# Kernel tuning notes

Measured on AMD Instinct MI355X. Metric: run time of the kernel, lower is better.

The kernel has to match this reference:

```python
import jax, jax.numpy as jnp
import numpy as np

EMBED_DIM = 1024
SEQ_LEN = 4096
NUM_HEADS = 16
HEAD_DIM = EMBED_DIM // NUM_HEADS
FREQ_BINS = SEQ_LEN // 2 + 1  # 2049
LN_EPS = 1e-5


def setup_inputs() -> dict:
    key = jax.random.key(0)
    ks = jax.random.split(key, 12)
    B = 4
    x = jax.random.normal(ks[0], (B, SEQ_LEN, EMBED_DIM), dtype=jnp.float32)
    # LayerNorm affine params
    ln_w = jnp.ones((EMBED_DIM,), dtype=jnp.float32)
    ln_b = jnp.zeros((EMBED_DIM,), dtype=jnp.float32)
    # spectral base filter / bias: (H, freq_bins, 1)
    base_filter = jax.random.normal(ks[1], (NUM_HEADS, FREQ_BINS, 1), dtype=jnp.float32)
    base_bias = jax.random.normal(ks[2], (NUM_HEADS, FREQ_BINS, 1), dtype=jnp.float32) - 0.1
    # adaptive MLP (depth=2, width=embed_dim): D -> D -> D -> H*freq*2, relu hidden
    out_size = NUM_HEADS * FREQ_BINS * 2
    s0 = 1.0 / np.sqrt(EMBED_DIM)
    w0 = jax.random.uniform(ks[3], (EMBED_DIM, EMBED_DIM), jnp.float32, -s0, s0)
    b0 = jax.random.uniform(ks[4], (EMBED_DIM,), jnp.float32, -s0, s0)
    w1 = jax.random.uniform(ks[5], (EMBED_DIM, EMBED_DIM), jnp.float32, -s0, s0)
    b1 = jax.random.uniform(ks[6], (EMBED_DIM,), jnp.float32, -s0, s0)
    w2 = jax.random.uniform(ks[7], (EMBED_DIM, out_size), jnp.float32, -s0, s0)
    b2 = jax.random.uniform(ks[8], (out_size,), jnp.float32, -s0, s0)
    return {"x": x, "ln_w": ln_w, "ln_b": ln_b,
            "base_filter": base_filter, "base_bias": base_bias,
            "w0": w0, "b0": b0, "w1": w1, "b1": b1, "w2": w2, "b2": b2}


def _complex_activation(z):
    mag = jnp.abs(z)
    scale = jax.nn.gelu(mag) / (mag + 1e-6)
    return z * scale


def reference(x, ln_w, ln_b, base_filter, base_bias, w0, b0, w1, b1, w2, b2):
    B, N, D = x.shape  # N == SEQ_LEN, D == EMBED_DIM
    # pre-norm LayerNorm over last dim
    mu = x.mean(axis=-1, keepdims=True)
    var = x.var(axis=-1, keepdims=True)
    x_norm = (x - mu) / jnp.sqrt(var + LN_EPS) * ln_w + ln_b
    # split heads: (B, H, N, head_dim)
    x_heads = x_norm.reshape(B, N, NUM_HEADS, HEAD_DIM).transpose(0, 2, 1, 3)
    F_fft = jnp.fft.rfft(x_heads, axis=2)  # (B, H, freq, head_dim), complex
    # adaptive params from mean-pooled context
    context = x_norm.mean(axis=1)  # (B, D)
    h = jax.nn.relu(context @ w0 + b0)
    h = jax.nn.relu(h @ w1 + b1)
    adapt = h @ w2 + b2  # (B, H*freq*2)
    adapt = adapt.reshape(B, NUM_HEADS, FREQ_BINS, 2)
    adaptive_scale = adapt[..., 0:1]
    adaptive_bias = adapt[..., 1:2]
    effective_filter = base_filter * (1.0 + adaptive_scale)  # (B, H, freq, 1)
    effective_bias = base_bias + adaptive_bias
    F_mod = F_fft * effective_filter + effective_bias
    F_nl = _complex_activation(F_mod)
    x_filt = jnp.fft.irfft(F_nl, n=SEQ_LEN, axis=2)  # (B, H, N, head_dim)
    x_filt = x_filt.transpose(0, 2, 1, 3).reshape(B, SEQ_LEN, EMBED_DIM)
    return x_filt  # dropout is identity (inference / rate 0)
```

## Files before the change

kernel.cpp:

```cpp
#include <hip/hip_runtime.h>
#include <hip/hip_fp16.h>
#include <math.h>

#define B_ 4
#define N_ 4096
#define D_ 1024
#define H_ 16
#define HD_ 64
#define FB_ 2049

typedef unsigned short ushort_t;
typedef unsigned int uint_t;

__device__ __forceinline__ float2 cmul(float2 a, float2 b) {
    return make_float2(a.x*b.x - a.y*b.y, a.x*b.y + a.y*b.x);
}
__device__ __forceinline__ float2 cadd(float2 a, float2 b){return make_float2(a.x+b.x,a.y+b.y);}
__device__ __forceinline__ float2 csub(float2 a, float2 b){return make_float2(a.x-b.x,a.y-b.y);}
__device__ __forceinline__ float2 cconj(float2 a){return make_float2(a.x,-a.y);}
__device__ __forceinline__ float2 addi(float2 a, float2 b){return make_float2(a.x-b.y, a.y+b.x);}
__device__ __forceinline__ float2 subi(float2 a, float2 b){return make_float2(a.x+b.y, a.y-b.x);}

__device__ __forceinline__ float gelu_t(float m) {
    float u = 0.7978845608028654f * (m + 0.044715f * m * m * m);
    float e = __expf(-2.0f * u);
    float th = (1.0f - e) / (1.0f + e);
    return 0.5f * m * (1.0f + th);
}
__device__ __forceinline__ float2 cact(float2 z) {
    float m = sqrtf(z.x*z.x + z.y*z.y);
    float s = gelu_t(m) / (m + 1e-6f);
    return make_float2(z.x*s, z.y*s);
}

__device__ __forceinline__ ushort_t f2h(float f) {
    __half h = __float2half_rn(f);
    return *reinterpret_cast<ushort_t*>(&h);
}
__device__ __forceinline__ float h2f(ushort_t u) {
    __half h = *reinterpret_cast<__half*>(&u);
    return __half2float(h);
}
__device__ __forceinline__ uint_t pk2(float a, float b) {
    return (uint_t)f2h(a) | ((uint_t)f2h(b) << 16);
}
__device__ __forceinline__ float lo_f(uint_t u){ return h2f((ushort_t)(u & 0xffffu)); }
__device__ __forceinline__ float hi_f(uint_t u){ return h2f((ushort_t)(u >> 16)); }

#define IX(e) ((e) + ((e) >> 4))

__device__ __forceinline__ int rev12(int p) {
    return ((p & 7) << 9) | (((p >> 3) & 7) << 6) | (((p >> 6) & 7) << 3) | ((p >> 9) & 7);
}

__global__ __launch_bounds__(256) void k_normT(const float* __restrict__ x,
                                               const float* __restrict__ lnw,
                                               const float* __restrict__ lnb,
                                               ushort_t* __restrict__ xt,
                                               float* __restrict__ cpart) {
    __shared__ ushort_t lds16[32 * 1032];
    uint_t* lds32 = (uint_t*)lds16;
    int blk = blockIdx.x;
    int b = blk >> 7, chunk = blk & 127;
    int n0 = chunk << 5;
    int lane = threadIdx.x & 63, w = threadIdx.x >> 6;
    const float4* lw4 = (const float4*)lnw;
    const float4* lb4 = (const float4*)lnb;
    float4 W0 = lw4[lane], W1 = lw4[lane+64], W2 = lw4[lane+128], W3 = lw4[lane+192];
    float4 G0 = lb4[lane], G1 = lb4[lane+64], G2 = lb4[lane+128], G3 = lb4[lane+192];

    for (int j = 0; j < 8; j++) {
        int r = (w << 3) + j;
        const float4* xr = (const float4*)(x + ((size_t)b * N_ + n0 + r) * D_);
        float4 v0 = xr[lane], v1 = xr[lane+64], v2 = xr[lane+128], v3 = xr[lane+192];
        float s = v0.x+v0.y+v0.z+v0.w + v1.x+v1.y+v1.z+v1.w
                + v2.x+v2.y+v2.z+v2.w + v3.x+v3.y+v3.z+v3.w;
        float q = v0.x*v0.x+v0.y*v0.y+v0.z*v0.z+v0.w*v0.w
                + v1.x*v1.x+v1.y*v1.y+v1.z*v1.z+v1.w*v1.w
                + v2.x*v2.x+v2.y*v2.y+v2.z*v2.z+v2.w*v2.w
                + v3.x*v3.x+v3.y*v3.y+v3.z*v3.z+v3.w*v3.w;
        for (int o = 1; o < 64; o <<= 1) { s += __shfl_xor(s, o); q += __shfl_xor(q, o); }
        float mu = s * (1.0f / D_);
        float rstd = rsqrtf(q * (1.0f / D_) - mu * mu + 1e-5f);
        int base = r * 516 + 2 * lane;
        lds32[base]       = pk2((v0.x-mu)*rstd*W0.x+G0.x, (v0.y-mu)*rstd*W0.y+G0.y);
        lds32[base + 1]   = pk2((v0.z-mu)*rstd*W0.z+G0.z, (v0.w-mu)*rstd*W0.w+G0.w);
        lds32[base + 128] = pk2((v1.x-mu)*rstd*W1.x+G1.x, (v1.y-mu)*rstd*W1.y+G1.y);
        lds32[base + 129] = pk2((v1.z-mu)*rstd*W1.z+G1.z, (v1.w-mu)*rstd*W1.w+G1.w);
        lds32[base + 256] = pk2((v2.x-mu)*rstd*W2.x+G2.x, (v2.y-mu)*rstd*W2.y+G2.y);
        lds32[base + 257] = pk2((v2.z-mu)*rstd*W2.z+G2.z, (v2.w-mu)*rstd*W2.w+G2.w);
        lds32[base + 384] = pk2((v3.x-mu)*rstd*W3.x+G3.x, (v3.y-mu)*rstd*W3.y+G3.y);
        lds32[base + 385] = pk2((v3.z-mu)*rstd*W3.z+G3.z, (v3.w-mu)*rstd*W3.w+G3.w);
    }
    __syncthreads();
    for (int half = 0; half < 2; half++) {
        int dp = threadIdx.x + (half << 8);
        float cs_e = 0.f, cs_o = 0.f;
        uint_t ce[16], co[16];
        #pragma unroll
        for (int i = 0; i < 16; i++) {
            uint_t w0 = lds32[(2*i) * 516 + dp];
            uint_t w1 = lds32[(2*i+1) * 516 + dp];
            ce[i] = (w0 & 0xffffu) | (w1 << 16);
            co[i] = (w0 >> 16) | (w1 & 0xffff0000u);
            cs_e += lo_f(w0) + lo_f(w1);
            cs_o += hi_f(w0) + hi_f(w1);
        }
        int de = dp * 2;
        uint4* dste = (uint4*)(xt + ((size_t)(b * 1024 + de)) * 4096 + n0);
        dste[0] = make_uint4(ce[0], ce[1], ce[2], ce[3]);
        dste[1] = make_uint4(ce[4], ce[5], ce[6], ce[7]);
        dste[2] = make_uint4(ce[8], ce[9], ce[10], ce[11]);
        dste[3] = make_uint4(ce[12], ce[13], ce[14], ce[15]);
        uint4* dsto = (uint4*)(xt + ((size_t)(b * 1024 + de + 1)) * 4096 + n0);
        dsto[0] = make_uint4(co[0], co[1], co[2], co[3]);
        dsto[1] = make_uint4(co[4], co[5], co[6], co[7]);
        dsto[2] = make_uint4(co[8], co[9], co[10], co[11]);
        dsto[3] = make_uint4(co[12], co[13], co[14], co[15]);
        ((float2*)(cpart + ((size_t)(b * 128 + chunk)) * D_))[dp] = make_float2(cs_e, cs_o);
    }
}

__global__ __launch_bounds__(256) void k_ctx(const float* __restrict__ cpart,
                                             float* __restrict__ ctx) {
    int id = blockIdx.x * 256 + threadIdx.x;
    int b = id >> 10, d = id & 1023;
    float s = 0.f;
    const float* p = cpart + (size_t)b * 128 * D_ + d;
    #pragma unroll 8
    for (int g = 0; g < 128; g++) s += p[g * D_];
    ctx[id] = s * (1.0f / N_);
}

__global__ __launch_bounds__(256) void k_mlp_part(const float* __restrict__ in,
                                                  const float* __restrict__ w,
                                                  float* __restrict__ part) {
    __shared__ float li[4 * 256];
    int ks = blockIdx.y;
    for (int i = threadIdx.x; i < 1024; i += 256) {
        int b = i >> 8, kk = i & 255;
        li[i] = in[b * 1024 + ks * 256 + kk];
    }
    __syncthreads();
    int col = blockIdx.x * 64 + (threadIdx.x & 63);
    int b = threadIdx.x >> 6;
    const float* wp = w + (size_t)(ks * 256) * 1024 + col;
    const float* ip = li + b * 256;
    float acc = 0.f;
    #pragma unroll 8
    for (int k = 0; k < 256; k++) acc = fmaf(ip[k], wp[(size_t)k * 1024], acc);
    part[((size_t)ks * 4 + b) * 1024 + col] = acc;
}

__global__ __launch_bounds__(256) void k_mlp_part2(const float* __restrict__ part,
                                                   const float* __restrict__ bias,
                                                   const float* __restrict__ w,
                                                   float* __restrict__ part2) {
    __shared__ float li[4 * 256];
    int ks = blockIdx.y;
    for (int i = threadIdx.x; i < 1024; i += 256) {
        int b = i >> 8, kk = (i & 255) + ks * 256;
        float v = part[b * 1024 + kk] + part[4096 + b * 1024 + kk] +
                  part[8192 + b * 1024 + kk] + part[12288 + b * 1024 + kk] + bias[kk];
        li[i] = fmaxf(v, 0.f);
    }
    __syncthreads();
    int col = blockIdx.x * 64 + (threadIdx.x & 63);
    int b = threadIdx.x >> 6;
    const float* wp = w + (size_t)(ks * 256) * 1024 + col;
    const float* ip = li + b * 256;
    float acc = 0.f;
    #pragma unroll 8
    for (int k = 0; k < 256; k++) acc = fmaf(ip[k], wp[(size_t)k * 1024], acc);
    part2[((size_t)ks * 4 + b) * 1024 + col] = acc;
}

__global__ __launch_bounds__(256) void k_adapt_part(const float* __restrict__ part2,
                                                    const float* __restrict__ b1,
                                                    const float* __restrict__ w2,
                                                    float* __restrict__ part3) {
    __shared__ float lh[4 * 128];
    int ks = blockIdx.y;
    for (int i = threadIdx.x; i < 512; i += 256) {
        int b = i >> 7, kk = (i & 127) + ks * 128;
        float v = part2[b * 1024 + kk] + part2[4096 + b * 1024 + kk] +
                  part2[8192 + b * 1024 + kk] + part2[12288 + b * 1024 + kk] + b1[kk];
        lh[i] = fmaxf(v, 0.f);
    }
    __syncthreads();
    int j4 = blockIdx.x * 1024 + threadIdx.x * 4;
    if (j4 < 65568) {
        float a0x=0,a0y=0,a0z=0,a0w=0, a1x=0,a1y=0,a1z=0,a1w=0;
        float a2x=0,a2y=0,a2z=0,a2w=0, a3x=0,a3y=0,a3z=0,a3w=0;
        const float* wp = w2 + (size_t)(ks * 128) * 65568 + j4;
        #pragma unroll 4
        for (int k = 0; k < 128; k++) {
            float4 wv = *(const float4*)(wp + (size_t)k * 65568);
            float h0 = lh[k], h1 = lh[128 + k], h2 = lh[256 + k], h3 = lh[384 + k];
            a0x = fmaf(h0, wv.x, a0x); a0y = fmaf(h0, wv.y, a0y);
            a0z = fmaf(h0, wv.z, a0z); a0w = fmaf(h0, wv.w, a0w);
            a1x = fmaf(h1, wv.x, a1x); a1y = fmaf(h1, wv.y, a1y);
            a1z = fmaf(h1, wv.z, a1z); a1w = fmaf(h1, wv.w, a1w);
            a2x = fmaf(h2, wv.x, a2x); a2y = fmaf(h2, wv.y, a2y);
            a2z = fmaf(h2, wv.z, a2z); a2w = fmaf(h2, wv.w, a2w);
            a3x = fmaf(h3, wv.x, a3x); a3y = fmaf(h3, wv.y, a3y);
            a3z = fmaf(h3, wv.z, a3z); a3w = fmaf(h3, wv.w, a3w);
        }
        float* p3 = part3 + (size_t)ks * 4 * 65568 + j4;
        *(float4*)(p3)              = make_float4(a0x, a0y, a0z, a0w);
        *(float4*)(p3 + 65568)      = make_float4(a1x, a1y, a1z, a1w);
        *(float4*)(p3 + 2 * 65568)  = make_float4(a2x, a2y, a2z, a2w);
        *(float4*)(p3 + 3 * 65568)  = make_float4(a3x, a3y, a3z, a3w);
    }
}

__global__ __launch_bounds__(256) void k_eff(const float* __restrict__ part3,
                                             const float* __restrict__ b2,
                                             const float* __restrict__ bfilt,
                                             const float* __restrict__ bbias,
                                             float2* __restrict__ eff) {
    int p = blockIdx.x * 256 + threadIdx.x;
    if (p >= 32784) return;
    int h = p / 2049, f = p % 2049;
    float bf = bfilt[p], bb = bbias[p];
    float sc0 = b2[2 * p], bi0 = b2[2 * p + 1];
    #pragma unroll
    for (int b = 0; b < 4; b++) {
        float sc = sc0, bi = bi0;
        #pragma unroll
        for (int s = 0; s < 8; s++) {
            const float* q = part3 + ((size_t)s * 4 + b) * 65568 + 2 * p;
            sc += q[0]; bi += q[1];
        }
        eff[((size_t)b * H_ + h) * FB_ + f] = make_float2(bf * (1.0f + sc), bb + bi);
    }
}

template<int M, int SH, bool TW>
__device__ __forceinline__ void dif_stage(float2* buf, const float2* tw, int t) {
    const float s2 = 0.70710678118654752f;
    int j = t & (M - 1);
    int base = 8 * t - 7 * j;
    float2 u0 = buf[IX(base)];
    float2 u1 = buf[IX(base + M)];
    float2 u2 = buf[IX(base + 2*M)];
    float2 u3 = buf[IX(base + 3*M)];
    float2 u4 = buf[IX(base + 4*M)];
    float2 u5 = buf[IX(base + 5*M)];
    float2 u6 = buf[IX(base + 6*M)];
    float2 u7 = buf[IX(base + 7*M)];
    float2 a0 = cadd(u0,u4), a1 = csub(u0,u4), a2 = cadd(u2,u6), a3 = csub(u2,u6);
    float2 E0 = cadd(a0,a2), E1 = subi(a1,a3), E2 = csub(a0,a2), E3 = addi(a1,a3);
    float2 c0 = cadd(u1,u5), c1 = csub(u1,u5), c2 = cadd(u3,u7), c3 = csub(u3,u7);
    float2 O0 = cadd(c0,c2), O1 = subi(c1,c3), O2 = csub(c0,c2), O3 = addi(c1,c3);
    float2 R1 = make_float2(s2*(O1.x + O1.y), s2*(O1.y - O1.x));
    float2 R2 = make_float2(O2.y, -O2.x);
    float2 R3 = make_float2(s2*(O3.y - O3.x), -s2*(O3.x + O3.y));
    float2 X0 = cadd(E0,O0), X4 = csub(E0,O0);
    float2 X1 = cadd(E1,R1), X5 = csub(E1,R1);
    float2 X2 = cadd(E2,R2), X6 = csub(E2,R2);
    float2 X3 = cadd(E3,R3), X7 = csub(E3,R3);
    buf[IX(base)] = X0;
    if (TW) {
        float2 w1 = tw[IX(j << SH)];
        float2 w = w1;
        buf[IX(base + M)]   = cmul(w, X1); w = cmul(w, w1);
        buf[IX(base + 2*M)] = cmul(w, X2); w = cmul(w, w1);
        buf[IX(base + 3*M)] = cmul(w, X3); w = cmul(w, w1);
        buf[IX(base + 4*M)] = cmul(w, X4); w = cmul(w, w1);
        buf[IX(base + 5*M)] = cmul(w, X5); w = cmul(w, w1);
        buf[IX(base + 6*M)] = cmul(w, X6); w = cmul(w, w1);
        buf[IX(base + 7*M)] = cmul(w, X7);
    } else {
        buf[IX(base + M)]   = X1;
        buf[IX(base + 2*M)] = X2;
        buf[IX(base + 3*M)] = X3;
        buf[IX(base + 4*M)] = X4;
        buf[IX(base + 5*M)] = X5;
        buf[IX(base + 6*M)] = X6;
        buf[IX(base + 7*M)] = X7;
    }
}

template<int M, int SH, bool TW>
__device__ __forceinline__ void dit_stage(float2* buf, const float2* tw, int t) {
    const float s2 = 0.70710678118654752f;
    int j = t & (M - 1);
    int base = 8 * t - 7 * j;
    float2 u0 = buf[IX(base)];
    float2 u1, u2, u3, u4, u5, u6, u7;
    if (TW) {
        float2 w1 = cconj(tw[IX(j << SH)]);
        float2 w = w1;
        u1 = cmul(w, buf[IX(base + M)]);   w = cmul(w, w1);
        u2 = cmul(w, buf[IX(base + 2*M)]); w = cmul(w, w1);
        u3 = cmul(w, buf[IX(base + 3*M)]); w = cmul(w, w1);
        u4 = cmul(w, buf[IX(base + 4*M)]); w = cmul(w, w1);
        u5 = cmul(w, buf[IX(base + 5*M)]); w = cmul(w, w1);
        u6 = cmul(w, buf[IX(base + 6*M)]); w = cmul(w, w1);
        u7 = cmul(w, buf[IX(base + 7*M)]);
    } else {
        u1 = buf[IX(base + M)];
        u2 = buf[IX(base + 2*M)];
        u3 = buf[IX(base + 3*M)];
        u4 = buf[IX(base + 4*M)];
        u5 = buf[IX(base + 5*M)];
        u6 = buf[IX(base + 6*M)];
        u7 = buf[IX(base + 7*M)];
    }
    float2 a0 = cadd(u0,u4), a1 = csub(u0,u4), a2 = cadd(u2,u6), a3 = csub(u2,u6);
    float2 E0 = cadd(a0,a2), E1 = addi(a1,a3), E2 = csub(a0,a2), E3 = subi(a1,a3);
    float2 c0 = cadd(u1,u5), c1 = csub(u1,u5), c2 = cadd(u3,u7), c3 = csub(u3,u7);
    float2 O0 = cadd(c0,c2), O1 = addi(c1,c3), O2 = csub(c0,c2), O3 = subi(c1,c3);
    float2 R1 = make_float2(s2*(O1.x - O1.y),  s2*(O1.x + O1.y));
    float2 R2 = make_float2(-O2.y, O2.x);
    float2 R3 = make_float2(-s2*(O3.x + O3.y), s2*(O3.x - O3.y));
    buf[IX(base)]       = cadd(E0,O0);
    buf[IX(base + 4*M)] = csub(E0,O0);
    buf[IX(base + M)]   = cadd(E1,R1);
    buf[IX(base + 5*M)] = csub(E1,R1);
    buf[IX(base + 2*M)] = cadd(E2,R2);
    buf[IX(base + 6*M)] = csub(E2,R2);
    buf[IX(base + 3*M)] = cadd(E3,R3);
    buf[IX(base + 7*M)] = csub(E3,R3);
}

__global__ __launch_bounds__(512, 6) void k_fftmod(ushort_t* __restrict__ xt,
                                                   const float2* __restrict__ eff) {
    __shared__ float2 buf[4352];
    __shared__ float2 tw[544];
    int t = threadIdx.x;
    int sig0 = blockIdx.x * 2;
    int b = sig0 >> 10;
    int h = (sig0 & 1023) >> 6;
    const float2* ef = eff + ((size_t)b * H_ + h) * FB_;
    ushort_t* xs = xt + (size_t)sig0 * 4096;

    {
        float sv, cv;
        __sincosf(-(float)M_PI * (float)t * (1.0f / 2048.0f), &sv, &cv);
        tw[IX(t)] = make_float2(cv, sv);
    }
    {
        const uint4* pa = (const uint4*)xs;
        const uint4* pb = pa + 512;
        uint4 ua = pa[t], ub = pb[t];
        int n = t << 3;
        buf[IX(n+0)] = make_float2(lo_f(ua.x), lo_f(ub.x));
        buf[IX(n+1)] = make_float2(hi_f(ua.x), hi_f(ub.x));
        buf[IX(n+2)] = make_float2(lo_f(ua.y), lo_f(ub.y));
        buf[IX(n+3)] = make_float2(hi_f(ua.y), hi_f(ub.y));
        buf[IX(n+4)] = make_float2(lo_f(ua.z), lo_f(ub.z));
        buf[IX(n+5)] = make_float2(hi_f(ua.z), hi_f(ub.z));
        buf[IX(n+6)] = make_float2(lo_f(ua.w), lo_f(ub.w));
        buf[IX(n+7)] = make_float2(hi_f(ua.w), hi_f(ub.w));
    }
    __syncthreads();

    dif_stage<512, 0, true >(buf, tw, t); __syncthreads();
    dif_stage<64,  3, true >(buf, tw, t); __syncthreads();
    dif_stage<8,   6, true >(buf, tw, t); __syncthreads();
    dif_stage<1,   0, false>(buf, tw, t); __syncthreads();

    if (t == 0) {
        float2 Z = buf[IX(0)];
        float2 e0 = ef[0];
        float Av = Z.x * e0.x + e0.y;
        float Bv = Z.y * e0.x + e0.y;
        float ma = fabsf(Av); Av *= gelu_t(ma) / (ma + 1e-6f);
        float mb = fabsf(Bv); Bv *= gelu_t(mb) / (mb + 1e-6f);
        buf[IX(0)] = make_float2(Av, Bv);
    }
    #pragma unroll
    for (int ii = 0; ii < 4; ii++) {
        int k = 1 + t + (ii << 9);
        if (k == 2048) {
            float2 Z = buf[IX(4)];
            float2 eN = ef[2048];
            float Av = Z.x * eN.x + eN.y;
            float Bv = Z.y * eN.x + eN.y;
            float ma = fabsf(Av); Av *= gelu_t(ma) / (ma + 1e-6f);
            float mb = fabsf(Bv); Bv *= gelu_t(mb) / (mb + 1e-6f);
            buf[IX(4)] = make_float2(Av, Bv);
        } else {
            int pk = rev12(k);
            int pq = rev12(4096 - k);
            float2 Zk = buf[IX(pk)], Zq = buf[IX(pq)];
            float2 A  = make_float2(0.5f*(Zk.x + Zq.x), 0.5f*(Zk.y - Zq.y));
            float2 Bc = make_float2(0.5f*(Zk.y + Zq.y), 0.5f*(Zq.x - Zk.x));
            float2 e = ef[k];
            float2 Ap = make_float2(A.x * e.x + e.y,  A.y * e.x);
            float2 Bp = make_float2(Bc.x * e.x + e.y, Bc.y * e.x);
            Ap = cact(Ap); Bp = cact(Bp);
            buf[IX(pk)] = make_float2(Ap.x - Bp.y, Ap.y + Bp.x);
            buf[IX(pq)] = make_float2(Ap.x + Bp.y, Bp.x - Ap.y);
        }
    }
    __syncthreads();

    dit_stage<1,   0, false>(buf, tw, t); __syncthreads();
    dit_stage<8,   6, true >(buf, tw, t); __syncthreads();
    dit_stage<64,  3, true >(buf, tw, t); __syncthreads();
    dit_stage<512, 0, true >(buf, tw, t); __syncthreads();

    {
        const float sc = 1.0f / 4096.0f;
        int n = t << 3;
        float2 z0 = buf[IX(n+0)], z1 = buf[IX(n+1)], z2 = buf[IX(n+2)], z3 = buf[IX(n+3)];
        float2 z4 = buf[IX(n+4)], z5 = buf[IX(n+5)], z6 = buf[IX(n+6)], z7 = buf[IX(n+7)];
        uint4 oa, ob;
        oa.x = pk2(z0.x*sc, z1.x*sc); oa.y = pk2(z2.x*sc, z3.x*sc);
        oa.z = pk2(z4.x*sc, z5.x*sc); oa.w = pk2(z6.x*sc, z7.x*sc);
        ob.x = pk2(z0.y*sc, z1.y*sc); ob.y = pk2(z2.y*sc, z3.y*sc);
        ob.z = pk2(z4.y*sc, z5.y*sc); ob.w = pk2(z6.y*sc, z7.y*sc);
        ((uint4*)xs)[t] = oa;
        ((uint4*)xs)[t + 512] = ob;
    }
}

__global__ __launch_bounds__(256) void k_transout(const ushort_t* __restrict__ xt,
                                                  float* __restrict__ out) {
    __shared__ float tile[64 * 65];
    int bid = blockIdx.x;
    int b = bid >> 10;
    int rem = bid & 1023;
    int nt = rem >> 4;
    int dt = rem & 15;
    int n0 = nt << 6;
    int tx = threadIdx.x & 63, ty = threadIdx.x >> 6;
    const ushort_t* xtb = xt + ((size_t)((b * H_ + dt) * HD_)) * (size_t)N_ + n0;
    for (int r = 0; r < 16; r++) {
        int dloc = ty + 4 * r;
        tile[dloc * 65 + tx] = h2f(xtb[(size_t)dloc * N_ + tx]);
    }
    __syncthreads();
    float* ob = out + ((size_t)b * N_ + n0) * D_ + dt * HD_;
    for (int r = 0; r < 16; r++) {
        int nn = ty + 4 * r;
        ob[(size_t)nn * D_ + tx] = tile[tx * 65 + nn];
    }
}

extern "C" void kernel_launch(void* const* d_in, const int* in_sizes, int n_in,
                              void* d_out, int out_size, void* d_ws, size_t ws_size,
                              hipStream_t stream) {
    const float* x     = (const float*)d_in[0];
    const float* lnw   = (const float*)d_in[1];
    const float* lnb   = (const float*)d_in[2];
    const float* bfilt = (const float*)d_in[3];
    const float* bbias = (const float*)d_in[4];
    const float* w0    = (const float*)d_in[5];
    const float* b0    = (const float*)d_in[6];
    const float* w1    = (const float*)d_in[7];
    const float* b1    = (const float*)d_in[8];
    const float* w2    = (const float*)d_in[9];
    const float* b2    = (const float*)d_in[10];

    float* ws = (float*)d_ws;
    ushort_t* xt   = (ushort_t*)ws;
    float*  cpart  = ws + 8388608;
    float*  ctx    = ws + 8912896;
    float*  pA     = ws + 8916992;
    float*  pB     = ws + 8933376;
    float*  p3     = ws + 8949760;
    float2* eff    = (float2*)(ws + 11047936);
    float*  out    = (float*)d_out;

    k_normT     <<<512,  256, 0, stream>>>(x, lnw, lnb, xt, cpart);
    k_ctx       <<<16,   256, 0, stream>>>(cpart, ctx);
    k_mlp_part  <<<dim3(16, 4), 256, 0, stream>>>(ctx, w0, pA);
    k_mlp_part2 <<<dim3(16, 4), 256, 0, stream>>>(pA, b0, w1, pB);
    k_adapt_part<<<dim3(65, 8), 256, 0, stream>>>(pB, b1, w2, p3);
    k_eff       <<<129,  256, 0, stream>>>(p3, b2, bfilt, bbias, eff);
    k_fftmod    <<<2048, 512, 0, stream>>>(xt, eff);
    k_transout  <<<4096, 256, 0, stream>>>(xt, out);
}
```

Before: 214.7 us.

## Shorten twiddle dependency chain and widen transpose-out tiles with vector loads

The FFT radix-8 stages now read both w and w^2 from a doubled twiddle table and derive the higher powers in a shallow tree instead of a serial chain of seven multiplies. This shortens the dependency chain and may limit error growth, at the cost of more shared memory and a lower occupancy hint. The output transpose kernel now handles 256x64 tiles per block, loading 16-byte vectors of half values into a padded shared tile and unpacking them on the way out. This is meant to cut the number of narrow global loads and launched blocks.

```diff
diff --git a/kernel.cpp b/kernel.cpp
--- a/kernel.cpp
+++ b/kernel.cpp
@@ -263,14 +263,19 @@
     buf[IX(base)] = X0;
     if (TW) {
         float2 w1 = tw[IX(j << SH)];
-        float2 w = w1;
-        buf[IX(base + M)]   = cmul(w, X1); w = cmul(w, w1);
-        buf[IX(base + 2*M)] = cmul(w, X2); w = cmul(w, w1);
-        buf[IX(base + 3*M)] = cmul(w, X3); w = cmul(w, w1);
-        buf[IX(base + 4*M)] = cmul(w, X4); w = cmul(w, w1);
-        buf[IX(base + 5*M)] = cmul(w, X5); w = cmul(w, w1);
-        buf[IX(base + 6*M)] = cmul(w, X6); w = cmul(w, w1);
-        buf[IX(base + 7*M)] = cmul(w, X7);
+        float2 w2 = tw[IX(j << (SH + 1))];
+        float2 w3 = cmul(w1, w2);
+        float2 w4 = cmul(w2, w2);
+        float2 w5 = cmul(w2, w3);
+        float2 w6 = cmul(w3, w3);
+        float2 w7 = cmul(w3, w4);
+        buf[IX(base + M)]   = cmul(w1, X1);
+        buf[IX(base + 2*M)] = cmul(w2, X2);
+        buf[IX(base + 3*M)] = cmul(w3, X3);
+        buf[IX(base + 4*M)] = cmul(w4, X4);
+        buf[IX(base + 5*M)] = cmul(w5, X5);
+        buf[IX(base + 6*M)] = cmul(w6, X6);
+        buf[IX(base + 7*M)] = cmul(w7, X7);
     } else {
         buf[IX(base + M)]   = X1;
         buf[IX(base + 2*M)] = X2;
@@ -291,14 +296,19 @@
     float2 u1, u2, u3, u4, u5, u6, u7;
     if (TW) {
         float2 w1 = cconj(tw[IX(j << SH)]);
-        float2 w = w1;
-        u1 = cmul(w, buf[IX(base + M)]);   w = cmul(w, w1);
-        u2 = cmul(w, buf[IX(base + 2*M)]); w = cmul(w, w1);
-        u3 = cmul(w, buf[IX(base + 3*M)]); w = cmul(w, w1);
-        u4 = cmul(w, buf[IX(base + 4*M)]); w = cmul(w, w1);
-        u5 = cmul(w, buf[IX(base + 5*M)]); w = cmul(w, w1);
-        u6 = cmul(w, buf[IX(base + 6*M)]); w = cmul(w, w1);
-        u7 = cmul(w, buf[IX(base + 7*M)]);
+        float2 w2 = cconj(tw[IX(j << (SH + 1))]);
+        float2 w3 = cmul(w1, w2);
+        float2 w4 = cmul(w2, w2);
+        float2 w5 = cmul(w2, w3);
+        float2 w6 = cmul(w3, w3);
+        float2 w7 = cmul(w3, w4);
+        u1 = cmul(w1, buf[IX(base + M)]);
+        u2 = cmul(w2, buf[IX(base + 2*M)]);
+        u3 = cmul(w3, buf[IX(base + 3*M)]);
+        u4 = cmul(w4, buf[IX(base + 4*M)]);
+        u5 = cmul(w5, buf[IX(base + 5*M)]);
+        u6 = cmul(w6, buf[IX(base + 6*M)]);
+        u7 = cmul(w7, buf[IX(base + 7*M)]);
     } else {
         u1 = buf[IX(base + M)];
         u2 = buf[IX(base + 2*M)];
@@ -325,10 +335,10 @@
     buf[IX(base + 7*M)] = csub(E3,R3);
 }
 
-__global__ __launch_bounds__(512, 6) void k_fftmod(ushort_t* __restrict__ xt,
+__global__ __launch_bounds__(512, 4) void k_fftmod(ushort_t* __restrict__ xt,
                                                    const float2* __restrict__ eff) {
     __shared__ float2 buf[4352];
-    __shared__ float2 tw[544];
+    __shared__ float2 tw[1088];
     int t = threadIdx.x;
     int sig0 = blockIdx.x * 2;
     int b = sig0 >> 10;
@@ -336,10 +346,12 @@
     const float2* ef = eff + ((size_t)b * H_ + h) * FB_;
     ushort_t* xs = xt + (size_t)sig0 * 4096;
 
-    {
+    #pragma unroll
+    for (int ii = 0; ii < 2; ii++) {
+        int e = t + (ii << 9);
         float sv, cv;
-        __sincosf(-(float)M_PI * (float)t * (1.0f / 2048.0f), &sv, &cv);
-        tw[IX(t)] = make_float2(cv, sv);
+        __sincosf(-(float)M_PI * (float)e * (1.0f / 2048.0f), &sv, &cv);
+        tw[IX(e)] = make_float2(cv, sv);
     }
     {
         const uint4* pa = (const uint4*)xs;
@@ -420,24 +432,33 @@
 
 __global__ __launch_bounds__(256) void k_transout(const ushort_t* __restrict__ xt,
                                                   float* __restrict__ out) {
-    __shared__ float tile[64 * 65];
+    __shared__ uint_t tile[64 * 133];
     int bid = blockIdx.x;
-    int b = bid >> 10;
-    int rem = bid & 1023;
+    int b = bid >> 8;
+    int rem = bid & 255;
     int nt = rem >> 4;
     int dt = rem & 15;
-    int n0 = nt << 6;
-    int tx = threadIdx.x & 63, ty = threadIdx.x >> 6;
-    const ushort_t* xtb = xt + ((size_t)((b * H_ + dt) * HD_)) * (size_t)N_ + n0;
-    for (int r = 0; r < 16; r++) {
-        int dloc = ty + 4 * r;
-        tile[dloc * 65 + tx] = h2f(xtb[(size_t)dloc * N_ + tx]);
-    }
-    __syncthreads();
-    float* ob = out + ((size_t)b * N_ + n0) * D_ + dt * HD_;
-    for (int r = 0; r < 16; r++) {
-        int nn = ty + 4 * r;
-        ob[(size_t)nn * D_ + tx] = tile[tx * 65 + nn];
+    int n0 = nt << 8, d0 = dt << 6;
+    int t = threadIdx.x;
+    const ushort_t* base = xt + ((size_t)(b * 1024 + d0)) * 4096 + n0;
+    #pragma unroll
+    for (int p = 0; p < 8; p++) {
+        int d = (p << 3) + (t >> 5);
+        int nc = (t & 31) << 3;
+        uint4 v = *(const uint4*)(base + (size_t)d * 4096 + nc);
+        uint_t* dst = tile + d * 133 + (nc >> 1);
+        dst[0] = v.x; dst[1] = v.y; dst[2] = v.z; dst[3] = v.w;
+    }
+    __syncthreads();
+    int d = t & 63;
+    int nq = t >> 6;
+    float* ob = out + ((size_t)b * N_ + n0) * D_ + d0 + d;
+    #pragma unroll 4
+    for (int i = 0; i < 64; i++) {
+        int n = (i << 2) + nq;
+        uint_t w = tile[d * 133 + (n >> 1)];
+        float v = (n & 1) ? hi_f(w) : lo_f(w);
+        ob[(size_t)n * D_] = v;
     }
 }
 
@@ -473,5 +494,5 @@
     k_adapt_part<<<dim3(65, 8), 256, 0, stream>>>(pB, b1, w2, p3);
     k_eff       <<<129,  256, 0, stream>>>(p3, b2, bfilt, bbias, eff);
     k_fftmod    <<<2048, 512, 0, stream>>>(xt, eff);
-    k_transout  <<<4096, 256, 0, stream>>>(xt, out);
-}
+    k_transout  <<<1024, 256, 0, stream>>>(xt, out);
+}
```

Result: slower. 219.3 us (+2.1%).
